# Kernel optimization log

Measured on AMD Instinct MI355X. Metric: run time of the kernel, lower is better.

Reference implementation:

```python
import jax, jax.numpy as jnp
import numpy as np
import math

D_MODEL = 2048
NUM_HEADS = 16
D_K = D_MODEL // NUM_HEADS  # 128
THETA = 10000.0
BATCH = 2
SEQ = 2048


def setup_inputs() -> dict:
    key = jax.random.key(0)
    k1, k2, k3 = jax.random.split(key, 3)
    std_qkv = math.sqrt(2.0 / (D_MODEL + 3 * D_MODEL))
    std_o = math.sqrt(2.0 / (D_MODEL + D_MODEL))
    return {
        "x": jax.random.normal(k1, (BATCH, SEQ, D_MODEL), dtype=jnp.float32),
        "token_positions": jnp.arange(SEQ, dtype=jnp.int64 if jax.config.jax_enable_x64 else jnp.int32),
        "Wqkv": jax.random.normal(k2, (3 * D_MODEL, D_MODEL), dtype=jnp.float32) * std_qkv,
        "Wo": jax.random.normal(k3, (D_MODEL, D_MODEL), dtype=jnp.float32) * std_o,
    }


def _rope(x, positions):
    # x: [b, h, t, d_k]; interleaved even/odd rotation as in the torch module
    half = D_K // 2
    inv_freq = 1.0 / (THETA ** (jnp.arange(half, dtype=x.dtype) / half))
    ang = positions.astype(x.dtype)[:, None] * inv_freq[None, :]  # [t, half]
    sin, cos = jnp.sin(ang), jnp.cos(ang)                          # broadcast over b,h
    x_even, x_odd = x[..., 0::2], x[..., 1::2]
    rot_even = x_even * cos - x_odd * sin
    rot_odd = x_even * sin + x_odd * cos
    return jnp.stack([rot_even, rot_odd], axis=-1).reshape(x.shape)


def reference(x, token_positions, Wqkv, Wo):
    B, T, _ = x.shape
    qkv = x @ Wqkv.T                                  # [b, t, 3*d_model]
    q, k, v = jnp.split(qkv, 3, axis=-1)
    def to_heads(t):
        return t.reshape(B, T, NUM_HEADS, D_K).transpose(0, 2, 1, 3)  # b h t d
    q, k, v = to_heads(q), to_heads(k), to_heads(v)
    q = _rope(q, token_positions)
    k = _rope(k, token_positions)
    scale = 1.0 / math.sqrt(D_K)
    scores = jnp.einsum("bhqd,bhkd->bhqk", q, k) * scale
    causal = jnp.tril(jnp.ones((T, T), dtype=bool))
    scores = jnp.where(causal, scores, jnp.finfo(scores.dtype).min)
    attn = jax.nn.softmax(scores, axis=-1)
    out = jnp.einsum("bhqk,bhkd->bhqd", attn, v)
    out = out.transpose(0, 2, 1, 3).reshape(B, T, D_MODEL)
    return out @ Wo.T
```

## Files before the change

### kernel.cpp

```cpp
#include <hip/hip_runtime.h>
#include <math.h>
#include <stdint.h>

#define NHEADS 16
#define DK 128
#define TSEQ 2048
#define DMODEL 2048

typedef __attribute__((ext_vector_type(8))) short short8;
typedef __attribute__((ext_vector_type(4))) float floatx4;

__device__ __forceinline__ float bf2f(unsigned short h) {
    return __uint_as_float(((unsigned int)h) << 16);
}
__device__ __forceinline__ unsigned short f2bf(float f) {
    unsigned int u = __float_as_uint(f);
    u += 0x7FFFu + ((u >> 16) & 1u);
    return (unsigned short)(u >> 16);
}
__device__ __forceinline__ void async16(unsigned short* lds, const unsigned short* g) {
    __builtin_amdgcn_global_load_lds(
        (const __attribute__((address_space(1))) uint32_t*)g,
        (__attribute__((address_space(3))) uint32_t*)lds, 16, 0, 0);
}

#define NX8 1048576
#define NW8 1572864
#define NO8 524288
__global__ __launch_bounds__(256) void cast_all_bf16(
    const float* __restrict__ x, const float* __restrict__ wqkv, const float* __restrict__ wo,
    unsigned short* __restrict__ xb, unsigned short* __restrict__ wqkvb, unsigned short* __restrict__ wob)
{
    const int i = blockIdx.x * 256 + threadIdx.x;
    const float* src; unsigned short* dst; int k;
    if (i < NX8)            { src = x;    dst = xb;    k = i; }
    else if (i < NX8 + NW8) { src = wqkv; dst = wqkvb; k = i - NX8; }
    else                    { src = wo;   dst = wob;   k = i - NX8 - NW8; }
    const float4* p4 = reinterpret_cast<const float4*>(src) + 2 * (size_t)k;
    const float4 a = p4[0], b = p4[1];
    uint32_t w0 = (uint32_t)f2bf(a.x) | ((uint32_t)f2bf(a.y) << 16);
    uint32_t w1 = (uint32_t)f2bf(a.z) | ((uint32_t)f2bf(a.w) << 16);
    uint32_t w2 = (uint32_t)f2bf(b.x) | ((uint32_t)f2bf(b.y) << 16);
    uint32_t w3 = (uint32_t)f2bf(b.z) | ((uint32_t)f2bf(b.w) << 16);
    uint4 o; o.x = w0; o.y = w1; o.z = w2; o.w = w3;
    *reinterpret_cast<uint4*>(dst + 8 * (size_t)k) = o;
}

__global__ __launch_bounds__(256) void rope_table_kernel(
    const int* __restrict__ pos, float2* __restrict__ tab)
{
    const int idx = blockIdx.x * 256 + threadIdx.x;
    const int tt = idx >> 6, i = idx & 63;
    const double inv_freq = exp(-log(10000.0) * (double)i / 64.0);
    const double ang = (double)pos[tt] * inv_freq;
    tab[idx] = make_float2((float)cos(ang), (float)sin(ang));
}

__global__ __launch_bounds__(512, 1) void gemm_qkv_8ph(
    const unsigned short* __restrict__ A, const unsigned short* __restrict__ B,
    unsigned short* __restrict__ qkvb, unsigned short* __restrict__ vt,
    const float2* __restrict__ tab)
{
    const int K = DMODEL, N = 3 * DMODEL;
    __shared__ unsigned short As[2][256 * 64];
    __shared__ unsigned short Bs[2][192 * 64];

    const int t = threadIdx.x;
    const int lane = t & 63, w = t >> 6;
    const int wr = w >> 2, wc = w & 3;
    const int lr = lane & 15, hi = lane >> 4;

    const int bid = (int)blockIdx.x;
    const int xcd = bid & 7, local = bid >> 3;
    const int row0 = (local & 15) * 256;
    const int col0 = ((xcd << 2) | (local >> 4)) * 192;

    const int rr = t >> 3;
    const int cc = ((t & 7) ^ (rr & 7)) << 3;
    const unsigned short* aP = A + (size_t)(row0 + rr) * K + cc;
    const unsigned short* bP = B + (size_t)(col0 + rr) * K + cc;
    const size_t rstep = (size_t)64 * K;

    floatx4 acc[8][3];
#pragma unroll
    for (int m = 0; m < 8; m++)
#pragma unroll
        for (int n = 0; n < 3; n++)
#pragma unroll
            for (int e = 0; e < 4; e++) acc[m][n][e] = 0.f;

#define STAGE(nb, k0n) do { \
        async16(&As[nb][t * 8],          aP + (k0n)); \
        async16(&As[nb][(t + 512) * 8],  aP + rstep + (k0n)); \
        async16(&As[nb][(t + 1024) * 8], aP + 2 * rstep + (k0n)); \
        async16(&As[nb][(t + 1536) * 8], aP + 3 * rstep + (k0n)); \
        async16(&Bs[nb][t * 8],          bP + (k0n)); \
        async16(&Bs[nb][(t + 512) * 8],  bP + rstep + (k0n)); \
        async16(&Bs[nb][(t + 1024) * 8], bP + 2 * rstep + (k0n)); \
    } while (0)

    STAGE(0, 0);
    const int NT = K >> 6;
    const int ch0 = (hi ^ (lr & 7)) * 8;
    const int ch1 = ((4 + hi) ^ (lr & 7)) * 8;

    short8 av[4][2], bv[3][2];

    for (int kt = 0; kt < NT; ++kt) {
        const int cur = kt & 1;
        const unsigned short* __restrict__ Ac = &As[cur][0];
        const unsigned short* __restrict__ Bc = &Bs[cur][0];

        if (kt + 1 < NT) {
            STAGE(cur ^ 1, (kt + 1) << 6);
            asm volatile("s_waitcnt vmcnt(7)" ::: "memory");
        } else {
            asm volatile("s_waitcnt vmcnt(0)" ::: "memory");
        }
        __builtin_amdgcn_s_barrier();
        __builtin_amdgcn_sched_barrier(0);

#pragma unroll
        for (int m = 0; m < 4; m++) {
            const int ar = (wr * 128 + m * 16 + lr) * 64;
            av[m][0] = *(const short8*)&Ac[ar + ch0];
            av[m][1] = *(const short8*)&Ac[ar + ch1];
        }
#pragma unroll
        for (int n = 0; n < 3; n++) {
            const int br = (wc * 48 + n * 16 + lr) * 64;
            bv[n][0] = *(const short8*)&Bc[br + ch0];
            bv[n][1] = *(const short8*)&Bc[br + ch1];
        }
        asm volatile("s_waitcnt lgkmcnt(0)" ::: "memory");
        __builtin_amdgcn_sched_barrier(0);
        __builtin_amdgcn_s_setprio(1);
#pragma unroll
        for (int m = 0; m < 4; m++)
#pragma unroll
            for (int n = 0; n < 3; n++) {
                acc[m][n] = __builtin_amdgcn_mfma_f32_16x16x32_bf16(av[m][0], bv[n][0], acc[m][n], 0, 0, 0);
                acc[m][n] = __builtin_amdgcn_mfma_f32_16x16x32_bf16(av[m][1], bv[n][1], acc[m][n], 0, 0, 0);
            }
        __builtin_amdgcn_s_setprio(0);
        __builtin_amdgcn_s_barrier();

#pragma unroll
        for (int m = 0; m < 4; m++) {
            const int ar = (wr * 128 + 64 + m * 16 + lr) * 64;
            av[m][0] = *(const short8*)&Ac[ar + ch0];
            av[m][1] = *(const short8*)&Ac[ar + ch1];
        }
        __builtin_amdgcn_s_barrier();
        asm volatile("s_waitcnt lgkmcnt(0)" ::: "memory");
        __builtin_amdgcn_sched_barrier(0);
        __builtin_amdgcn_s_setprio(1);
#pragma unroll
        for (int m = 0; m < 4; m++)
#pragma unroll
            for (int n = 0; n < 3; n++) {
                acc[4 + m][n] = __builtin_amdgcn_mfma_f32_16x16x32_bf16(av[m][0], bv[n][0], acc[4 + m][n], 0, 0, 0);
                acc[4 + m][n] = __builtin_amdgcn_mfma_f32_16x16x32_bf16(av[m][1], bv[n][1], acc[4 + m][n], 0, 0, 0);
            }
        __builtin_amdgcn_s_setprio(0);
        __builtin_amdgcn_s_barrier();
    }
#undef STAGE

    const int par = lr & 1;
#pragma unroll
    for (int mi = 0; mi < 8; mi++) {
        const int row = row0 + wr * 128 + mi * 16 + hi * 4;
        const int tt = row & (TSEQ - 1);
        const int bb = row >> 11;
#pragma unroll
        for (int ni = 0; ni < 3; ni++) {
            const int col = col0 + wc * 48 + ni * 16 + lr;
            if (col < 2 * DMODEL) {
                const int pi = (col & 127) >> 1;
#pragma unroll
                for (int j = 0; j < 4; j++) {
                    const float2 cs = tab[(tt + j) * 64 + pi];
                    const float v = acc[mi][ni][j];
                    const float p = __shfl_xor(v, 1, 64);
                    const float o = par ? (p * cs.y + v * cs.x)
                                        : (v * cs.x - p * cs.y);
                    qkvb[(size_t)(row + j) * N + col] = f2bf(o);
                }
            } else {
                const int vcol = col - 2 * DMODEL;
                const int h = vcol >> 7, d = vcol & 127;
                uint2 pw;
                pw.x = (uint32_t)f2bf(acc[mi][ni][0]) | ((uint32_t)f2bf(acc[mi][ni][1]) << 16);
                pw.y = (uint32_t)f2bf(acc[mi][ni][2]) | ((uint32_t)f2bf(acc[mi][ni][3]) << 16);
                *(uint2*)&vt[(size_t)((bb * NHEADS + h) * DK + d) * TSEQ + tt] = pw;
            }
        }
    }
}

template<int OUT_BF16>
__global__ __launch_bounds__(256) void gemm_bt_bf16(
    const unsigned short* __restrict__ A, const unsigned short* __restrict__ B,
    void* __restrict__ Cv, int M, int N, int K)
{
    __shared__ unsigned short As[128 * 32];
    __shared__ unsigned short Bs[128 * 32];

    const int t = threadIdx.x;
    const int lane = t & 63, w = t >> 6;
    const int row0 = blockIdx.y * 128, col0 = blockIdx.x * 128;
    const int wr = (w >> 1) * 64, wc = (w & 1) * 64;
    const int lr = lane & 15, lk = lane >> 4;

    floatx4 acc[4][4];
#pragma unroll
    for (int i = 0; i < 4; i++)
#pragma unroll
        for (int j = 0; j < 4; j++)
#pragma unroll
            for (int e = 0; e < 4; e++) acc[i][j][e] = 0.f;

    const int c0 = w * 64 + lane, c1 = c0 + 256;
    const size_t ga0 = (size_t)(row0 + (c0 >> 2)) * K + ((c0 & 3) << 3);
    const size_t ga1 = (size_t)(row0 + (c1 >> 2)) * K + ((c1 & 3) << 3);
    const size_t gb0 = (size_t)(col0 + (c0 >> 2)) * K + ((c0 & 3) << 3);
    const size_t gb1 = (size_t)(col0 + (c1 >> 2)) * K + ((c1 & 3) << 3);

    for (int k0 = 0; k0 < K; k0 += 32) {
        async16(&As[c0 * 8], A + ga0 + k0);
        async16(&As[c1 * 8], A + ga1 + k0);
        async16(&Bs[c0 * 8], B + gb0 + k0);
        async16(&Bs[c1 * 8], B + gb1 + k0);
        __syncthreads();

        short8 a[4], b[4];
#pragma unroll
        for (int mi = 0; mi < 4; mi++)
            a[mi] = *(const short8*)&As[(wr + mi * 16 + lr) * 32 + lk * 8];
#pragma unroll
        for (int ni = 0; ni < 4; ni++)
            b[ni] = *(const short8*)&Bs[(wc + ni * 16 + lr) * 32 + lk * 8];
#pragma unroll
        for (int mi = 0; mi < 4; mi++)
#pragma unroll
            for (int ni = 0; ni < 4; ni++)
                acc[mi][ni] = __builtin_amdgcn_mfma_f32_16x16x32_bf16(
                    a[mi], b[ni], acc[mi][ni], 0, 0, 0);
        __syncthreads();
    }

#pragma unroll
    for (int mi = 0; mi < 4; mi++)
#pragma unroll
        for (int ni = 0; ni < 4; ni++) {
            const int colb = col0 + wc + ni * 16 + lr;
#pragma unroll
            for (int j = 0; j < 4; j++) {
                const int rowb = row0 + wr + mi * 16 + lk * 4 + j;
                if (OUT_BF16)
                    ((unsigned short*)Cv)[(size_t)rowb * N + colb] = f2bf(acc[mi][ni][j]);
                else
                    ((float*)Cv)[(size_t)rowb * N + colb] = acc[mi][ni][j];
            }
        }
}

__global__ __launch_bounds__(256, 2) void attn_mfma2_kernel(
    const unsigned short* __restrict__ qkvb, const unsigned short* __restrict__ vt,
    unsigned short* __restrict__ outb)
{
    __shared__ unsigned short Ks[2][64 * 128];
    __shared__ unsigned short Vs[128 * 64];
    __shared__ unsigned short Ps[4][32 * 64];

    const int t = threadIdx.x;
    const int lane = t & 63, w = t >> 6;
    const int lr = lane & 15, hi = lane >> 4;
    const int bh = blockIdx.y, b = bh >> 4, h = bh & 15;
    const int qc = (int)gridDim.x - 1 - (int)blockIdx.x;
    const int q0 = qc * 128;
    const int q0w = q0 + w * 32;
    const float scale = 0.08838834764831845f;
    const size_t QROW = 3 * DMODEL;

    const unsigned short* kg = qkvb + (size_t)b * TSEQ * QROW + DMODEL + h * DK;
    const unsigned short* vg = vt + (size_t)bh * DK * TSEQ;

    short8 qf[2][4];
    {
        const unsigned short* qbase = qkvb + (size_t)(b * TSEQ + q0w) * QROW + h * DK;
#pragma unroll
        for (int nt = 0; nt < 2; nt++)
#pragma unroll
            for (int ks = 0; ks < 4; ks++) {
                short8 raw = *(const short8*)(qbase + (size_t)(nt * 16 + lr) * QROW + ks * 32 + hi * 8);
                short8 sc;
#pragma unroll
                for (int e = 0; e < 8; e++)
                    sc[e] = (short)f2bf(bf2f((unsigned short)raw[e]) * scale);
                qf[nt][ks] = sc;
            }
    }

    auto stageK = [&](int bufi, int kv0s) {
#pragma unroll
        for (int i = 0; i < 4; i++) {
            const int s = i * 256 + t;
            const int r = s >> 4;
            const int cc = (s & 15) ^ (r & 7);
            async16(&Ks[bufi][s * 8], kg + (size_t)(kv0s + r) * QROW + cc * 8);
        }
    };
    auto stageV = [&](int kv0s) {
#pragma unroll
        for (int i = 0; i < 4; i++) {
            const int s = i * 256 + t;
            const int r = s >> 3;
            const int cc = (s & 7) ^ (r & 7);
            async16(&Vs[s * 8], vg + (size_t)r * TSEQ + kv0s + cc * 8);
        }
    };

    floatx4 accO[2][8];
#pragma unroll
    for (int nt = 0; nt < 2; nt++)
#pragma unroll
        for (int dt = 0; dt < 8; dt++)
#pragma unroll
            for (int e = 0; e < 4; e++) accO[nt][dt][e] = 0.f;
    float mrun[2] = {-1e30f, -1e30f};
    float lrun[2] = {0.f, 0.f};

    const int ntiles = (q0 + 128) / 64;
    int kbuf = 0;

    stageK(0, 0);
    __syncthreads();

    const int pswz = (lr & 7) << 1;

    for (int ti = 0; ti < ntiles; ti++) {
        const int kv0 = ti * 64;
        stageV(kv0);
        if (ti + 1 < ntiles) stageK(kbuf ^ 1, kv0 + 64);

        const bool active = (kv0 <= q0w + 31);
        float al[2] = {1.f, 1.f};

        if (active) {
            floatx4 st[4][2];
#pragma unroll
            for (int mt = 0; mt < 4; mt++)
#pragma unroll
                for (int nt = 0; nt < 2; nt++)
#pragma unroll
                    for (int e = 0; e < 4; e++) st[mt][nt][e] = 0.f;
#pragma unroll
            for (int mt = 0; mt < 4; mt++) {
                const int r = mt * 16 + lr;
#pragma unroll
                for (int ks = 0; ks < 4; ks++) {
                    const int ch = (ks * 4 + hi) ^ (r & 7);
                    const short8 kf = *(const short8*)&Ks[kbuf][(r * 16 + ch) * 8];
                    st[mt][0] = __builtin_amdgcn_mfma_f32_16x16x32_bf16(kf, qf[0][ks], st[mt][0], 0, 0, 0);
                    st[mt][1] = __builtin_amdgcn_mfma_f32_16x16x32_bf16(kf, qf[1][ks], st[mt][1], 0, 0, 0);
                }
            }
            if (kv0 + 63 > q0w) {
#pragma unroll
                for (int nt = 0; nt < 2; nt++) {
                    const int qg = q0w + nt * 16 + lr;
#pragma unroll
                    for (int mt = 0; mt < 4; mt++)
#pragma unroll
                        for (int rg = 0; rg < 4; rg++) {
                            const int kvg = kv0 + mt * 16 + hi * 4 + rg;
                            if (kvg > qg) st[mt][nt][rg] = -1e30f;
                        }
                }
            }
            float pm[2];
#pragma unroll
            for (int nt = 0; nt < 2; nt++) {
                float m = -1e30f;
#pragma unroll
                for (int mt = 0; mt < 4; mt++)
#pragma unroll
                    for (int rg = 0; rg < 4; rg++) m = fmaxf(m, st[mt][nt][rg]);
                m = fmaxf(m, __shfl_xor(m, 16, 64));
                m = fmaxf(m, __shfl_xor(m, 32, 64));
                pm[nt] = m;
            }
            if (__any((pm[0] > mrun[0] + 8.f) || (pm[1] > mrun[1] + 8.f))) {
#pragma unroll
                for (int nt = 0; nt < 2; nt++) {
                    const float mn = fmaxf(mrun[nt], pm[nt]);
                    al[nt] = __expf(mrun[nt] - mn);
                    mrun[nt] = mn;
                }
#pragma unroll
                for (int rg = 0; rg < 4; rg++) {
                    const float a0 = __shfl(al[0], hi * 4 + rg, 64);
                    const float a1 = __shfl(al[1], hi * 4 + rg, 64);
#pragma unroll
                    for (int dt = 0; dt < 8; dt++) {
                        accO[0][dt][rg] *= a0;
                        accO[1][dt][rg] *= a1;
                    }
                }
            }
#pragma unroll
            for (int nt = 0; nt < 2; nt++) {
                float ls = 0.f;
                const int prow = nt * 16 + lr;
#pragma unroll
                for (int mt = 0; mt < 4; mt++) {
                    float pv[4];
#pragma unroll
                    for (int rg = 0; rg < 4; rg++) {
                        pv[rg] = __expf(st[mt][nt][rg] - mrun[nt]);
                        ls += pv[rg];
                    }
                    uint2 pw;
                    pw.x = (uint32_t)f2bf(pv[0]) | ((uint32_t)f2bf(pv[1]) << 16);
                    pw.y = (uint32_t)f2bf(pv[2]) | ((uint32_t)f2bf(pv[3]) << 16);
                    const int chunk = (mt * 4 + hi) ^ pswz;
                    *(uint2*)&Ps[w][prow * 64 + chunk * 4] = pw;
                }
                ls += __shfl_xor(ls, 16, 64);
                ls += __shfl_xor(ls, 32, 64);
                lrun[nt] = lrun[nt] * al[nt] + ls;
            }
        }
        __syncthreads();

        if (active) {
#pragma unroll
            for (int ks2 = 0; ks2 < 2; ks2++) {
                const int ch0 = ((ks2 * 8 + hi * 2) ^ pswz) * 4;
                const short8 pa0 = *(const short8*)&Ps[w][(0 * 16 + lr) * 64 + ch0];
                const short8 pa1 = *(const short8*)&Ps[w][(1 * 16 + lr) * 64 + ch0];
#pragma unroll
                for (int dt = 0; dt < 8; dt++) {
                    const int r = dt * 16 + lr;
                    const int ch = (ks2 * 4 + hi) ^ (r & 7);
                    const short8 vf = *(const short8*)&Vs[(r * 8 + ch) * 8];
                    accO[0][dt] = __builtin_amdgcn_mfma_f32_16x16x32_bf16(pa0, vf, accO[0][dt], 0, 0, 0);
                    accO[1][dt] = __builtin_amdgcn_mfma_f32_16x16x32_bf16(pa1, vf, accO[1][dt], 0, 0, 0);
                }
            }
        }
        __syncthreads();
        kbuf ^= 1;
    }

#pragma unroll
    for (int nt = 0; nt < 2; nt++) {
        const float lv_own = 1.f / lrun[nt];
#pragma unroll
        for (int rg = 0; rg < 4; rg++) {
            const float lv = __shfl(lv_own, hi * 4 + rg, 64);
            unsigned short* orow = outb + (size_t)(b * TSEQ + q0w + nt * 16 + hi * 4 + rg) * DMODEL + h * DK;
#pragma unroll
            for (int dt = 0; dt < 8; dt++)
                orow[dt * 16 + lr] = f2bf(accO[nt][dt][rg] * lv);
        }
    }
}

extern "C" void kernel_launch(void* const* d_in, const int* in_sizes, int n_in,
                              void* d_out, int out_size, void* d_ws, size_t ws_size,
                              hipStream_t stream)
{
    const float* x    = (const float*)d_in[0];
    const int*   pos  = (const int*)d_in[1];
    const float* Wqkv = (const float*)d_in[2];
    const float* Wo   = (const float*)d_in[3];
    float* out = (float*)d_out;

    unsigned short* qkvb  = (unsigned short*)d_ws;
    unsigned short* vtb   = qkvb + (size_t)25165824;
    unsigned short* xb    = vtb + (size_t)8388608;
    unsigned short* attnb = xb;
    unsigned short* wqkvb = xb + (size_t)8388608;
    unsigned short* wob   = wqkvb + (size_t)12582912;
    float2* tab = (float2*)(wob + (size_t)4194304);

    const int M = 2 * TSEQ;

    cast_all_bf16<<<12288, 256, 0, stream>>>(x, Wqkv, Wo, xb, wqkvb, wob);
    rope_table_kernel<<<512, 256, 0, stream>>>(pos, tab);

    gemm_qkv_8ph<<<dim3(512), 512, 0, stream>>>(xb, wqkvb, qkvb, vtb, tab);

    attn_mfma2_kernel<<<dim3(16, 32), 256, 0, stream>>>(qkvb, vtb, attnb);

    gemm_bt_bf16<0><<<dim3(16, 32), 256, 0, stream>>>(attnb, wob, (void*)out, M, DMODEL, DMODEL);
}
```

Baseline: 298.8 us.

## Replace output GEMM with pipelined 8-wave kernel and refine load/barrier waits

Swaps the simple 128x128 single-buffered output projection GEMM for a 256x128 tile, 512-thread, double-buffered kernel with swizzled LDS and XCD-aware block mapping. It also splits B-tile staging in the QKV GEMM so it is issued between the two MFMA phases. In attention, the block barriers are replaced with explicit vmcnt waits plus s_barrier. These target the memory stalls and synchronisation cost of the old output GEMM and the prefetch timing elsewhere, at the risk of incorrect wait counts or lower occupancy.

```diff
diff --git a/kernel.cpp b/kernel.cpp
--- a/kernel.cpp
+++ b/kernel.cpp
@@ -89,6 +89,153 @@
 #pragma unroll
             for (int e = 0; e < 4; e++) acc[m][n][e] = 0.f;
 
+#define STAGE_A(nb, k0n) do { \
+        async16(&As[nb][t * 8],          aP + (k0n)); \
+        async16(&As[nb][(t + 512) * 8],  aP + rstep + (k0n)); \
+        async16(&As[nb][(t + 1024) * 8], aP + 2 * rstep + (k0n)); \
+        async16(&As[nb][(t + 1536) * 8], aP + 3 * rstep + (k0n)); \
+    } while (0)
+#define STAGE_B(nb, k0n) do { \
+        async16(&Bs[nb][t * 8],          bP + (k0n)); \
+        async16(&Bs[nb][(t + 512) * 8],  bP + rstep + (k0n)); \
+        async16(&Bs[nb][(t + 1024) * 8], bP + 2 * rstep + (k0n)); \
+    } while (0)
+
+    STAGE_A(0, 0);
+    STAGE_B(0, 0);
+    const int NT = K >> 6;
+    const int ch0 = (hi ^ (lr & 7)) * 8;
+    const int ch1 = ((4 + hi) ^ (lr & 7)) * 8;
+
+    short8 av[4][2], bv[3][2];
+
+    for (int kt = 0; kt < NT; ++kt) {
+        const int cur = kt & 1;
+        const unsigned short* __restrict__ Ac = &As[cur][0];
+        const unsigned short* __restrict__ Bc = &Bs[cur][0];
+
+        if (kt + 1 < NT) {
+            STAGE_A(cur ^ 1, (kt + 1) << 6);
+            asm volatile("s_waitcnt vmcnt(4)" ::: "memory");
+        } else {
+            asm volatile("s_waitcnt vmcnt(0)" ::: "memory");
+        }
+        __builtin_amdgcn_s_barrier();
+        __builtin_amdgcn_sched_barrier(0);
+
+#pragma unroll
+        for (int m = 0; m < 4; m++) {
+            const int ar = (wr * 128 + m * 16 + lr) * 64;
+            av[m][0] = *(const short8*)&Ac[ar + ch0];
+            av[m][1] = *(const short8*)&Ac[ar + ch1];
+        }
+#pragma unroll
+        for (int n = 0; n < 3; n++) {
+            const int br = (wc * 48 + n * 16 + lr) * 64;
+            bv[n][0] = *(const short8*)&Bc[br + ch0];
+            bv[n][1] = *(const short8*)&Bc[br + ch1];
+        }
+        asm volatile("s_waitcnt lgkmcnt(0)" ::: "memory");
+        __builtin_amdgcn_sched_barrier(0);
+        __builtin_amdgcn_s_setprio(1);
+#pragma unroll
+        for (int m = 0; m < 4; m++)
+#pragma unroll
+            for (int n = 0; n < 3; n++) {
+                acc[m][n] = __builtin_amdgcn_mfma_f32_16x16x32_bf16(av[m][0], bv[n][0], acc[m][n], 0, 0, 0);
+                acc[m][n] = __builtin_amdgcn_mfma_f32_16x16x32_bf16(av[m][1], bv[n][1], acc[m][n], 0, 0, 0);
+            }
+        __builtin_amdgcn_s_setprio(0);
+        __builtin_amdgcn_s_barrier();
+
+        if (kt + 1 < NT) STAGE_B(cur ^ 1, (kt + 1) << 6);
+#pragma unroll
+        for (int m = 0; m < 4; m++) {
+            const int ar = (wr * 128 + 64 + m * 16 + lr) * 64;
+            av[m][0] = *(const short8*)&Ac[ar + ch0];
+            av[m][1] = *(const short8*)&Ac[ar + ch1];
+        }
+        __builtin_amdgcn_s_barrier();
+        asm volatile("s_waitcnt lgkmcnt(0)" ::: "memory");
+        __builtin_amdgcn_sched_barrier(0);
+        __builtin_amdgcn_s_setprio(1);
+#pragma unroll
+        for (int m = 0; m < 4; m++)
+#pragma unroll
+            for (int n = 0; n < 3; n++) {
+                acc[4 + m][n] = __builtin_amdgcn_mfma_f32_16x16x32_bf16(av[m][0], bv[n][0], acc[4 + m][n], 0, 0, 0);
+                acc[4 + m][n] = __builtin_amdgcn_mfma_f32_16x16x32_bf16(av[m][1], bv[n][1], acc[4 + m][n], 0, 0, 0);
+            }
+        __builtin_amdgcn_s_setprio(0);
+        __builtin_amdgcn_s_barrier();
+    }
+#undef STAGE_A
+#undef STAGE_B
+
+    const int par = lr & 1;
+#pragma unroll
+    for (int mi = 0; mi < 8; mi++) {
+        const int row = row0 + wr * 128 + mi * 16 + hi * 4;
+        const int tt = row & (TSEQ - 1);
+        const int bb = row >> 11;
+#pragma unroll
+        for (int ni = 0; ni < 3; ni++) {
+            const int col = col0 + wc * 48 + ni * 16 + lr;
+            if (col < 2 * DMODEL) {
+                const int pi = (col & 127) >> 1;
+#pragma unroll
+                for (int j = 0; j < 4; j++) {
+                    const float2 cs = tab[(tt + j) * 64 + pi];
+                    const float v = acc[mi][ni][j];
+                    const float p = __shfl_xor(v, 1, 64);
+                    const float o = par ? (p * cs.y + v * cs.x)
+                                        : (v * cs.x - p * cs.y);
+                    qkvb[(size_t)(row + j) * N + col] = f2bf(o);
+                }
+            } else {
+                const int vcol = col - 2 * DMODEL;
+                const int h = vcol >> 7, d = vcol & 127;
+                uint2 pw;
+                pw.x = (uint32_t)f2bf(acc[mi][ni][0]) | ((uint32_t)f2bf(acc[mi][ni][1]) << 16);
+                pw.y = (uint32_t)f2bf(acc[mi][ni][2]) | ((uint32_t)f2bf(acc[mi][ni][3]) << 16);
+                *(uint2*)&vt[(size_t)((bb * NHEADS + h) * DK + d) * TSEQ + tt] = pw;
+            }
+        }
+    }
+}
+
+__global__ __launch_bounds__(512, 1) void gemm_o_8ph(
+    const unsigned short* __restrict__ A, const unsigned short* __restrict__ B,
+    float* __restrict__ C)
+{
+    const int K = DMODEL, N = DMODEL;
+    __shared__ unsigned short As[2][256 * 64];
+    __shared__ unsigned short Bs[2][128 * 64];
+
+    const int t = threadIdx.x;
+    const int lane = t & 63, w = t >> 6;
+    const int wr = w >> 2, wc = w & 3;
+    const int lr = lane & 15, hi = lane >> 4;
+
+    const int bid = (int)blockIdx.x;
+    const int xcd = bid & 7, local = bid >> 3;
+    const int row0 = (local & 15) * 256;
+    const int col0 = ((xcd << 1) | (local >> 4)) * 128;
+
+    const int rr = t >> 3;
+    const int cc = ((t & 7) ^ (rr & 7)) << 3;
+    const unsigned short* aP = A + (size_t)(row0 + rr) * K + cc;
+    const unsigned short* bP = B + (size_t)(col0 + rr) * K + cc;
+    const size_t rstep = (size_t)64 * K;
+
+    floatx4 acc[8][2];
+#pragma unroll
+    for (int m = 0; m < 8; m++)
+#pragma unroll
+        for (int n = 0; n < 2; n++)
+#pragma unroll
+            for (int e = 0; e < 4; e++) acc[m][n][e] = 0.f;
+
 #define STAGE(nb, k0n) do { \
         async16(&As[nb][t * 8],          aP + (k0n)); \
         async16(&As[nb][(t + 512) * 8],  aP + rstep + (k0n)); \
@@ -96,7 +243,6 @@
         async16(&As[nb][(t + 1536) * 8], aP + 3 * rstep + (k0n)); \
         async16(&Bs[nb][t * 8],          bP + (k0n)); \
         async16(&Bs[nb][(t + 512) * 8],  bP + rstep + (k0n)); \
-        async16(&Bs[nb][(t + 1024) * 8], bP + 2 * rstep + (k0n)); \
     } while (0)
 
     STAGE(0, 0);
@@ -104,7 +250,7 @@
     const int ch0 = (hi ^ (lr & 7)) * 8;
     const int ch1 = ((4 + hi) ^ (lr & 7)) * 8;
 
-    short8 av[4][2], bv[3][2];
+    short8 av[4][2], bv[2][2];
 
     for (int kt = 0; kt < NT; ++kt) {
         const int cur = kt & 1;
@@ -113,7 +259,7 @@
 
         if (kt + 1 < NT) {
             STAGE(cur ^ 1, (kt + 1) << 6);
-            asm volatile("s_waitcnt vmcnt(7)" ::: "memory");
+            asm volatile("s_waitcnt vmcnt(6)" ::: "memory");
         } else {
             asm volatile("s_waitcnt vmcnt(0)" ::: "memory");
         }
@@ -127,8 +273,8 @@
             av[m][1] = *(const short8*)&Ac[ar + ch1];
         }
 #pragma unroll
-        for (int n = 0; n < 3; n++) {
-            const int br = (wc * 48 + n * 16 + lr) * 64;
+        for (int n = 0; n < 2; n++) {
+            const int br = (wc * 32 + n * 16 + lr) * 64;
             bv[n][0] = *(const short8*)&Bc[br + ch0];
             bv[n][1] = *(const short8*)&Bc[br + ch1];
         }
@@ -138,7 +284,7 @@
 #pragma unroll
         for (int m = 0; m < 4; m++)
 #pragma unroll
-            for (int n = 0; n < 3; n++) {
+            for (int n = 0; n < 2; n++) {
                 acc[m][n] = __builtin_amdgcn_mfma_f32_16x16x32_bf16(av[m][0], bv[n][0], acc[m][n], 0, 0, 0);
                 acc[m][n] = __builtin_amdgcn_mfma_f32_16x16x32_bf16(av[m][1], bv[n][1], acc[m][n], 0, 0, 0);
             }
@@ -158,7 +304,7 @@
 #pragma unroll
         for (int m = 0; m < 4; m++)
 #pragma unroll
-            for (int n = 0; n < 3; n++) {
+            for (int n = 0; n < 2; n++) {
                 acc[4 + m][n] = __builtin_amdgcn_mfma_f32_16x16x32_bf16(av[m][0], bv[n][0], acc[4 + m][n], 0, 0, 0);
                 acc[4 + m][n] = __builtin_amdgcn_mfma_f32_16x16x32_bf16(av[m][1], bv[n][1], acc[4 + m][n], 0, 0, 0);
             }
@@ -167,103 +313,17 @@
     }
 #undef STAGE
 
-    const int par = lr & 1;
 #pragma unroll
     for (int mi = 0; mi < 8; mi++) {
         const int row = row0 + wr * 128 + mi * 16 + hi * 4;
-        const int tt = row & (TSEQ - 1);
-        const int bb = row >> 11;
-#pragma unroll
-        for (int ni = 0; ni < 3; ni++) {
-            const int col = col0 + wc * 48 + ni * 16 + lr;
-            if (col < 2 * DMODEL) {
-                const int pi = (col & 127) >> 1;
-#pragma unroll
-                for (int j = 0; j < 4; j++) {
-                    const float2 cs = tab[(tt + j) * 64 + pi];
-                    const float v = acc[mi][ni][j];
-                    const float p = __shfl_xor(v, 1, 64);
-                    const float o = par ? (p * cs.y + v * cs.x)
-                                        : (v * cs.x - p * cs.y);
-                    qkvb[(size_t)(row + j) * N + col] = f2bf(o);
-                }
-            } else {
-                const int vcol = col - 2 * DMODEL;
-                const int h = vcol >> 7, d = vcol & 127;
-                uint2 pw;
-                pw.x = (uint32_t)f2bf(acc[mi][ni][0]) | ((uint32_t)f2bf(acc[mi][ni][1]) << 16);
-                pw.y = (uint32_t)f2bf(acc[mi][ni][2]) | ((uint32_t)f2bf(acc[mi][ni][3]) << 16);
-                *(uint2*)&vt[(size_t)((bb * NHEADS + h) * DK + d) * TSEQ + tt] = pw;
-            }
-        }
-    }
-}
-
-template<int OUT_BF16>
-__global__ __launch_bounds__(256) void gemm_bt_bf16(
-    const unsigned short* __restrict__ A, const unsigned short* __restrict__ B,
-    void* __restrict__ Cv, int M, int N, int K)
-{
-    __shared__ unsigned short As[128 * 32];
-    __shared__ unsigned short Bs[128 * 32];
-
-    const int t = threadIdx.x;
-    const int lane = t & 63, w = t >> 6;
-    const int row0 = blockIdx.y * 128, col0 = blockIdx.x * 128;
-    const int wr = (w >> 1) * 64, wc = (w & 1) * 64;
-    const int lr = lane & 15, lk = lane >> 4;
-
-    floatx4 acc[4][4];
-#pragma unroll
-    for (int i = 0; i < 4; i++)
-#pragma unroll
-        for (int j = 0; j < 4; j++)
-#pragma unroll
-            for (int e = 0; e < 4; e++) acc[i][j][e] = 0.f;
-
-    const int c0 = w * 64 + lane, c1 = c0 + 256;
-    const size_t ga0 = (size_t)(row0 + (c0 >> 2)) * K + ((c0 & 3) << 3);
-    const size_t ga1 = (size_t)(row0 + (c1 >> 2)) * K + ((c1 & 3) << 3);
-    const size_t gb0 = (size_t)(col0 + (c0 >> 2)) * K + ((c0 & 3) << 3);
-    const size_t gb1 = (size_t)(col0 + (c1 >> 2)) * K + ((c1 & 3) << 3);
-
-    for (int k0 = 0; k0 < K; k0 += 32) {
-        async16(&As[c0 * 8], A + ga0 + k0);
-        async16(&As[c1 * 8], A + ga1 + k0);
-        async16(&Bs[c0 * 8], B + gb0 + k0);
-        async16(&Bs[c1 * 8], B + gb1 + k0);
-        __syncthreads();
-
-        short8 a[4], b[4];
-#pragma unroll
-        for (int mi = 0; mi < 4; mi++)
-            a[mi] = *(const short8*)&As[(wr + mi * 16 + lr) * 32 + lk * 8];
-#pragma unroll
-        for (int ni = 0; ni < 4; ni++)
-            b[ni] = *(const short8*)&Bs[(wc + ni * 16 + lr) * 32 + lk * 8];
-#pragma unroll
-        for (int mi = 0; mi < 4; mi++)
-#pragma unroll
-            for (int ni = 0; ni < 4; ni++)
-                acc[mi][ni] = __builtin_amdgcn_mfma_f32_16x16x32_bf16(
-                    a[mi], b[ni], acc[mi][ni], 0, 0, 0);
-        __syncthreads();
-    }
-
-#pragma unroll
-    for (int mi = 0; mi < 4; mi++)
-#pragma unroll
-        for (int ni = 0; ni < 4; ni++) {
-            const int colb = col0 + wc + ni * 16 + lr;
-#pragma unroll
-            for (int j = 0; j < 4; j++) {
-                const int rowb = row0 + wr + mi * 16 + lk * 4 + j;
-                if (OUT_BF16)
-                    ((unsigned short*)Cv)[(size_t)rowb * N + colb] = f2bf(acc[mi][ni][j]);
-                else
-                    ((float*)Cv)[(size_t)rowb * N + colb] = acc[mi][ni][j];
-            }
-        }
+#pragma unroll
+        for (int ni = 0; ni < 2; ni++) {
+            const int col = col0 + wc * 32 + ni * 16 + lr;
+#pragma unroll
+            for (int j = 0; j < 4; j++)
+                C[(size_t)(row + j) * N + col] = acc[mi][ni][j];
+        }
+    }
 }
 
 __global__ __launch_bounds__(256, 2) void attn_mfma2_kernel(
@@ -342,8 +402,9 @@
 
     for (int ti = 0; ti < ntiles; ti++) {
         const int kv0 = ti * 64;
+        const bool havK = (ti + 1 < ntiles);
         stageV(kv0);
-        if (ti + 1 < ntiles) stageK(kbuf ^ 1, kv0 + 64);
+        if (havK) stageK(kbuf ^ 1, kv0 + 64);
 
         const bool active = (kv0 <= q0w + 31);
         float al[2] = {1.f, 1.f};
@@ -433,7 +494,9 @@
                 lrun[nt] = lrun[nt] * al[nt] + ls;
             }
         }
-        __syncthreads();
+        if (havK) asm volatile("s_waitcnt vmcnt(4)" ::: "memory");
+        else      asm volatile("s_waitcnt vmcnt(0)" ::: "memory");
+        __builtin_amdgcn_s_barrier();
 
         if (active) {
 #pragma unroll
@@ -451,7 +514,8 @@
                 }
             }
         }
-        __syncthreads();
+        asm volatile("s_waitcnt vmcnt(0)" ::: "memory");
+        __builtin_amdgcn_s_barrier();
         kbuf ^= 1;
     }
 
@@ -487,8 +551,6 @@
     unsigned short* wob   = wqkvb + (size_t)12582912;
     float2* tab = (float2*)(wob + (size_t)4194304);
 
-    const int M = 2 * TSEQ;
-
     cast_all_bf16<<<12288, 256, 0, stream>>>(x, Wqkv, Wo, xb, wqkvb, wob);
     rope_table_kernel<<<512, 256, 0, stream>>>(pos, tab);
 
@@ -496,5 +558,5 @@
 
     attn_mfma2_kernel<<<dim3(16, 32), 256, 0, stream>>>(qkvb, vtb, attnb);
 
-    gemm_bt_bf16<0><<<dim3(16, 32), 256, 0, stream>>>(attnb, wob, (void*)out, M, DMODEL, DMODEL);
-}
+    gemm_o_8ph<<<dim3(256), 512, 0, stream>>>(attnb, wob, out);
+}
```

New measurement: 285.8 us. 4.4% less time.
